# Performance work log

Hardware: AMD Instinct MI355X
Metric: run time of the kernel (lower is better)

The kernel has to match this reference:

```python
import jax, jax.numpy as jnp
import numpy as np

N = 100000
E = 3200000
D = 256


def setup_inputs() -> dict:
    key = jax.random.key(0)
    k1, k2, k3, k4 = jax.random.split(key, 4)
    x = jax.random.normal(k1, (N, D), dtype=jnp.float32)
    edge_index = jax.random.randint(k2, (2, E), 0, N, dtype=jnp.int64)
    # Glorot-ish scale for weights
    s = 1.0 / np.sqrt(D)
    W1 = jax.random.normal(k3, (D, D), dtype=jnp.float32) * s
    W2 = jax.random.normal(k4, (D, D), dtype=jnp.float32) * s
    b1 = jnp.zeros((D,), dtype=jnp.float32)
    b2 = jnp.zeros((D,), dtype=jnp.float32)
    return {"x": x, "edge_index": edge_index, "W1": W1, "b1": b1, "W2": W2, "b2": b2}


def _gcn_norm(edge_index, num_nodes):
    # PyG gcn_norm with add_self_loops=True, symmetric normalization.
    loop = jnp.arange(num_nodes, dtype=edge_index.dtype)
    src = jnp.concatenate([edge_index[0], loop])  # [E+N]
    dst = jnp.concatenate([edge_index[1], loop])  # [E+N]
    ones = jnp.ones(src.shape[0], dtype=jnp.float32)
    deg = jax.ops.segment_sum(ones, dst, num_segments=num_nodes)  # in-degree incl. self loop
    dis = jnp.where(deg > 0, jax.lax.rsqrt(deg), 0.0)
    norm = dis[src] * dis[dst]  # [E+N]
    return src, dst, norm


def _gcn_layer(x, src, dst, norm, W, b, num_nodes):
    xw = x @ W                                   # [N, D] dense GEMM
    msg = xw[src] * norm[:, None]                # gather + scale  [E+N, D]
    out = jax.ops.segment_sum(msg, dst, num_segments=num_nodes)  # scatter-add
    return out + b


def reference(x, edge_index, W1, b1, W2, b2):
    src, dst, norm = _gcn_norm(edge_index, N)
    h = jax.nn.elu(_gcn_layer(x, src, dst, norm, W1, b1, N))
    h = jax.nn.elu(_gcn_layer(h, src, dst, norm, W2, b2, N))
    return h
```

## Files before the change

kernel.cpp:

```cpp
#include <hip/hip_runtime.h>
#include <math.h>

#define N_NODES 100000
#define N_EDGES 3200000
#define DIM 256
#define SCAN_B 1024
#define SCAN_NBLK ((N_NODES + SCAN_B - 1) / SCAN_B)
#define NPASS 8
#define WIN ((N_NODES + NPASS - 1) / NPASS)

typedef unsigned short u16;
typedef unsigned int u32;
typedef __attribute__((ext_vector_type(8))) short bf16x8;
typedef __attribute__((ext_vector_type(4))) float f32x4;

__device__ __forceinline__ float bf2f(u16 u) {
    union { u32 i; float f; } v; v.i = ((u32)u) << 16; return v.f;
}
__device__ __forceinline__ u16 f2bf(float f) {
    union { float f; u32 i; } v; v.f = f;
    u32 x = v.i;
    return (u16)((x + 0x7fffu + ((x >> 16) & 1u)) >> 16);
}
__device__ __forceinline__ float sane(float v) {
    union { float f; u32 i; } u; u.f = v;
    if ((u.i & 0x7f800000u) == 0x7f800000u) return 0.f;
    return v;
}
__device__ __forceinline__ int iclamp(int v, int lo, int hi) {
    return v < lo ? lo : (v > hi ? hi : v);
}

__global__ void detect_kernel(const u32* __restrict__ xw_words,
                              const int* __restrict__ ei, int* __restrict__ flags) {
    int lane = threadIdx.x;
    int cnt = 0;
#pragma unroll
    for (int j = 0; j < 4; ++j) {
        u32 e = (xw_words[lane + 64 * j] >> 7) & 0xffu;
        cnt += (e >= 0x70 && e <= 0x88) ? 1 : 0;
    }
    int nz = 0;
#pragma unroll
    for (int j = 0; j < 4; ++j) nz += (ei[2 * (lane + 64 * j) + 1] != 0) ? 1 : 0;
#pragma unroll
    for (int off = 32; off; off >>= 1) {
        cnt += __shfl_down(cnt, off, 64);
        nz += __shfl_down(nz, off, 64);
    }
    if (lane == 0) {
        flags[0] = (cnt < 128) ? 1 : 0;
        flags[1] = (nz == 0) ? 1 : 0;
    }
}

__device__ __forceinline__ int edge_val(const int* __restrict__ ei, int which,
                                        int i, int f64) {
    long long idx = (long long)which * N_EDGES + i;
    int v = f64 ? ei[idx * 2] : ei[idx];
    return iclamp(v, 0, N_NODES - 1);
}

__global__ void convert_x(const void* __restrict__ xin, u16* __restrict__ xbf,
                          const int* __restrict__ flags) {
    long long i = (long long)blockIdx.x * blockDim.x + threadIdx.x;
    if (i >= (long long)N_NODES * DIM) return;
    float v = flags[0] ? ((const float*)xin)[i] : bf2f(((const u16*)xin)[i]);
    xbf[i] = f2bf(sane(v));
}

__global__ void count_convert(const int* __restrict__ ei, int* __restrict__ rowcount,
                              int* __restrict__ src32, int* __restrict__ dst32,
                              const int* __restrict__ flags) {
    int i = blockIdx.x * blockDim.x + threadIdx.x;
    if (i < N_EDGES) {
        int f = flags[1];
        int s = edge_val(ei, 0, i, f);
        int d = edge_val(ei, 1, i, f);
        src32[i] = s;
        dst32[i] = d;
        atomicAdd(&rowcount[d], 1);
    }
}

__global__ void compute_dis(const int* __restrict__ rowcount, float* __restrict__ dis) {
    int i = blockIdx.x * blockDim.x + threadIdx.x;
    if (i < N_NODES) {
        int c = iclamp(rowcount[i], 0, N_EDGES);
        dis[i] = rsqrtf((float)(c + 1));
    }
}

__global__ __launch_bounds__(SCAN_B) void scan_block_sums(const int* __restrict__ cnt,
                                                          int* __restrict__ bsum) {
    __shared__ int ws[16];
    int i = blockIdx.x * SCAN_B + threadIdx.x;
    int v = (i < N_NODES) ? cnt[i] : 0;
#pragma unroll
    for (int off = 32; off; off >>= 1) v += __shfl_down(v, off, 64);
    if ((threadIdx.x & 63) == 0) ws[threadIdx.x >> 6] = v;
    __syncthreads();
    if (threadIdx.x < 16) {
        int t = ws[threadIdx.x];
#pragma unroll
        for (int off = 8; off; off >>= 1) t += __shfl_down(t, off, 16);
        if (threadIdx.x == 0) bsum[blockIdx.x] = t;
    }
}

__global__ void scan_bsum(int* __restrict__ bsum, int* __restrict__ rowptr) {
    __shared__ int sdata[128];
    int i = threadIdx.x;
    int v = (i < SCAN_NBLK) ? bsum[i] : 0;
    sdata[i] = v;
    __syncthreads();
    for (int off = 1; off < 128; off <<= 1) {
        int t = (i >= off) ? sdata[i - off] : 0;
        __syncthreads();
        sdata[i] += t;
        __syncthreads();
    }
    if (i < SCAN_NBLK) bsum[i] = sdata[i] - v;
    if (i == 0) rowptr[N_NODES] = sdata[127];
}

__global__ __launch_bounds__(SCAN_B) void scan_final(const int* __restrict__ cnt,
                                                     const int* __restrict__ bsum,
                                                     int* __restrict__ rowptr,
                                                     int* __restrict__ cursor) {
    __shared__ int ws[16];
    int lane = threadIdx.x & 63;
    int wid = threadIdx.x >> 6;
    int i = blockIdx.x * SCAN_B + threadIdx.x;
    int c = (i < N_NODES) ? cnt[i] : 0;
    int v = c;
#pragma unroll
    for (int off = 1; off < 64; off <<= 1) {
        int t = __shfl_up(v, off, 64);
        if (lane >= off) v += t;
    }
    if (lane == 63) ws[wid] = v;
    __syncthreads();
    int woff = 0;
    for (int w = 0; w < wid; ++w) woff += ws[w];
    int excl = bsum[blockIdx.x] + woff + v - c;
    if (i < N_NODES) { rowptr[i] = excl; cursor[i] = excl; }
}

__global__ void fill_csr_pass(const int* __restrict__ src32,
                              const int* __restrict__ dst32,
                              int* __restrict__ cursor, int* __restrict__ colidx,
                              int lo) {
    int i = blockIdx.x * blockDim.x + threadIdx.x;
    if (i < N_EDGES) {
        int d = dst32[i];
        if ((unsigned)(d - lo) < (unsigned)WIN) {
            int pos = atomicAdd(&cursor[d], 1);
            colidx[pos] = src32[i];
        }
    }
}

__global__ void transpose_w(const void* __restrict__ W, u16* __restrict__ Wt,
                            const int* __restrict__ flags) {
    int n = blockIdx.x;
    int k = threadIdx.x;
    float v = flags[0] ? ((const float*)W)[k * DIM + n]
                       : bf2f(((const u16*)W)[k * DIM + n]);
    Wt[n * DIM + k] = f2bf(sane(v));
}

__global__ __launch_bounds__(256) void gemm_mfma(const u16* __restrict__ A,
                                                 const u16* __restrict__ Wt,
                                                 u16* __restrict__ out) {
    int w = threadIdx.x >> 6;
    int lane = threadIdx.x & 63;
    int rt = blockIdx.x;
    int m = lane & 15;
    int quad = lane >> 4;

    bf16x8 B[4][8];
#pragma unroll
    for (int t2 = 0; t2 < 4; ++t2)
#pragma unroll
        for (int ks = 0; ks < 8; ++ks)
            B[t2][ks] = *(const bf16x8*)(Wt + (size_t)((w * 4 + t2) * 16 + m) * DIM +
                                         ks * 32 + quad * 8);

    const u16* arow = A + (size_t)(rt * 16 + m) * DIM + quad * 8;
    f32x4 acc[4];
#pragma unroll
    for (int t2 = 0; t2 < 4; ++t2) acc[t2] = (f32x4){0.f, 0.f, 0.f, 0.f};

#pragma unroll
    for (int ks = 0; ks < 8; ++ks) {
        bf16x8 a = *(const bf16x8*)(arow + ks * 32);
#pragma unroll
        for (int t2 = 0; t2 < 4; ++t2)
            acc[t2] = __builtin_amdgcn_mfma_f32_16x16x32_bf16(a, B[t2][ks], acc[t2], 0, 0, 0);
    }

#pragma unroll
    for (int t2 = 0; t2 < 4; ++t2) {
#pragma unroll
        for (int r = 0; r < 4; ++r) {
            int row = rt * 16 + quad * 4 + r;
            int c = w * 64 + t2 * 16 + m;
            out[(size_t)row * DIM + c] = f2bf(sane(acc[t2][r]));
        }
    }
}

__global__ __launch_bounds__(256) void aggregate(const u16* __restrict__ xw,
                                                 const int* __restrict__ rowptr,
                                                 const int* __restrict__ colidx,
                                                 const float* __restrict__ dis,
                                                 const void* __restrict__ bias,
                                                 void* __restrict__ out,
                                                 const int* __restrict__ flags,
                                                 int final_layer) {
    int wid = threadIdx.x >> 6;
    int lane = threadIdx.x & 63;
    int node = blockIdx.x * 4 + wid;
    if (node >= N_NODES) return;
    int c0 = lane * 4;
    const u16* base = xw + c0;

    float dn = dis[node];
    float a0, a1, a2, a3;
    {
        ushort4 v = *(const ushort4*)(base + (size_t)node * DIM);
        a0 = dn * bf2f(v.x); a1 = dn * bf2f(v.y);
        a2 = dn * bf2f(v.z); a3 = dn * bf2f(v.w);
    }
    int beg = rowptr[node];
    int end = rowptr[node + 1];
    int e = beg;
    for (; e + 8 <= end; e += 8) {
        int s[8];
        float w[8];
        ushort4 vv[8];
#pragma unroll
        for (int k = 0; k < 8; ++k) s[k] = colidx[e + k];
#pragma unroll
        for (int k = 0; k < 8; ++k) vv[k] = *(const ushort4*)(base + (size_t)s[k] * DIM);
#pragma unroll
        for (int k = 0; k < 8; ++k) w[k] = dis[s[k]];
#pragma unroll
        for (int k = 0; k < 8; ++k) {
            a0 += w[k] * bf2f(vv[k].x);
            a1 += w[k] * bf2f(vv[k].y);
            a2 += w[k] * bf2f(vv[k].z);
            a3 += w[k] * bf2f(vv[k].w);
        }
    }
    for (; e < end; ++e) {
        int s = colidx[e];
        float w = dis[s];
        ushort4 v = *(const ushort4*)(base + (size_t)s * DIM);
        a0 += w * bf2f(v.x); a1 += w * bf2f(v.y);
        a2 += w * bf2f(v.z); a3 += w * bf2f(v.w);
    }

    float b0, b1, b2, b3;
    int f32mode = flags[0];
    if (f32mode) {
        float4 bv = *(const float4*)((const float*)bias + c0);
        b0 = bv.x; b1 = bv.y; b2 = bv.z; b3 = bv.w;
    } else {
        ushort4 bv = *(const ushort4*)((const u16*)bias + c0);
        b0 = bf2f(bv.x); b1 = bf2f(bv.y); b2 = bf2f(bv.z); b3 = bf2f(bv.w);
    }
    float o0 = dn * a0 + b0;
    float o1 = dn * a1 + b1;
    float o2 = dn * a2 + b2;
    float o3 = dn * a3 + b3;
    o0 = sane(o0 > 0.f ? o0 : expm1f(o0));
    o1 = sane(o1 > 0.f ? o1 : expm1f(o1));
    o2 = sane(o2 > 0.f ? o2 : expm1f(o2));
    o3 = sane(o3 > 0.f ? o3 : expm1f(o3));
    if (final_layer && f32mode) {
        float4 ov; ov.x = o0; ov.y = o1; ov.z = o2; ov.w = o3;
        *(float4*)((float*)out + (size_t)node * DIM + c0) = ov;
    } else {
        ushort4 ov;
        ov.x = f2bf(o0); ov.y = f2bf(o1); ov.z = f2bf(o2); ov.w = f2bf(o3);
        *(ushort4*)((u16*)out + (size_t)node * DIM + c0) = ov;
    }
}

extern "C" void kernel_launch(void* const* d_in, const int* in_sizes, int n_in,
                              void* d_out, int out_size, void* d_ws, size_t ws_size,
                              hipStream_t stream) {
    const void* x  = d_in[0];
    const int*  ei = (const int*)d_in[1];
    const void* W1 = d_in[2];
    const void* b1 = d_in[3];
    const void* W2 = d_in[4];
    const void* b2 = d_in[5];

    char* ws = (char*)d_ws;
    size_t off = 0;
    auto alloc = [&](size_t bytes) {
        void* p = ws + off;
        off = (off + bytes + 255) & ~(size_t)255;
        return p;
    };
    int*   flags    = (int*)alloc(256);
    int*   rowcount = (int*)alloc((size_t)N_NODES * 4);
    int*   rowptr   = (int*)alloc((size_t)(N_NODES + 1) * 4);
    int*   cursor   = (int*)alloc((size_t)N_NODES * 4);
    int*   colidx   = (int*)alloc((size_t)N_EDGES * 4);
    float* dis      = (float*)alloc((size_t)N_NODES * 4);
    int*   bsum     = (int*)alloc((size_t)SCAN_NBLK * 4 + 256);
    u16*   Wt       = (u16*)alloc((size_t)DIM * DIM * 2);
    u16*   xw       = (u16*)alloc((size_t)N_NODES * DIM * 2);
    (void)ws_size;

    int* src32 = (int*)xw;
    int* dst32 = src32 + N_EDGES;

    u16* xbf = (u16*)d_out;

    detect_kernel<<<1, 64, 0, stream>>>((const u32*)x, ei, flags);
    hipMemsetAsync(rowcount, 0, (size_t)N_NODES * 4, stream);
    count_convert<<<(N_EDGES + 255) / 256, 256, 0, stream>>>(ei, rowcount, src32, dst32, flags);
    compute_dis<<<(N_NODES + 255) / 256, 256, 0, stream>>>(rowcount, dis);
    scan_block_sums<<<SCAN_NBLK, SCAN_B, 0, stream>>>(rowcount, bsum);
    scan_bsum<<<1, 128, 0, stream>>>(bsum, rowptr);
    scan_final<<<SCAN_NBLK, SCAN_B, 0, stream>>>(rowcount, bsum, rowptr, cursor);
    for (int p = 0; p < NPASS; ++p)
        fill_csr_pass<<<(N_EDGES + 255) / 256, 256, 0, stream>>>(src32, dst32, cursor,
                                                                 colidx, p * WIN);
    convert_x<<<(N_NODES * DIM + 255) / 256, 256, 0, stream>>>(x, xbf, flags);

    transpose_w<<<DIM, DIM, 0, stream>>>(W1, Wt, flags);
    gemm_mfma<<<N_NODES / 16, 256, 0, stream>>>(xbf, Wt, xw);
    aggregate<<<N_NODES / 4, 256, 0, stream>>>(xw, rowptr, colidx, dis, b1, d_out, flags, 0);

    transpose_w<<<DIM, DIM, 0, stream>>>(W2, Wt, flags);
    gemm_mfma<<<N_NODES / 16, 256, 0, stream>>>((const u16*)d_out, Wt, xw);
    aggregate<<<N_NODES / 4, 256, 0, stream>>>(xw, rowptr, colidx, dis, b2, d_out, flags, 1);
}
```

Before: 1.235 ms.

## Prescale GEMM output by source norm and split wave across edges in aggregate

```diff
diff --git a/kernel.cpp b/kernel.cpp
--- a/kernel.cpp
+++ b/kernel.cpp
@@ -29,6 +29,12 @@
 }
 __device__ __forceinline__ int iclamp(int v, int lo, int hi) {
     return v < lo ? lo : (v > hi ? hi : v);
+}
+__device__ __forceinline__ float2 cvt2(u32 d) {
+    union { u32 i; float f; } lo, hi;
+    lo.i = d << 16;
+    hi.i = d & 0xffff0000u;
+    return make_float2(lo.f, hi.f);
 }
 
 __global__ void detect_kernel(const u32* __restrict__ xw_words,
@@ -172,6 +178,7 @@
 
 __global__ __launch_bounds__(256) void gemm_mfma(const u16* __restrict__ A,
                                                  const u16* __restrict__ Wt,
+                                                 const float* __restrict__ dis,
                                                  u16* __restrict__ out) {
     int w = threadIdx.x >> 6;
     int lane = threadIdx.x & 63;
@@ -200,13 +207,16 @@
             acc[t2] = __builtin_amdgcn_mfma_f32_16x16x32_bf16(a, B[t2][ks], acc[t2], 0, 0, 0);
     }
 
+    float4 dv = *(const float4*)(dis + rt * 16 + quad * 4);
+    float dr[4] = {dv.x, dv.y, dv.z, dv.w};
+
 #pragma unroll
     for (int t2 = 0; t2 < 4; ++t2) {
 #pragma unroll
         for (int r = 0; r < 4; ++r) {
             int row = rt * 16 + quad * 4 + r;
             int c = w * 64 + t2 * 16 + m;
-            out[(size_t)row * DIM + c] = f2bf(sane(acc[t2][r]));
+            out[(size_t)row * DIM + c] = f2bf(sane(acc[t2][r] * dr[r]));
         }
     }
 }
@@ -223,45 +233,72 @@
     int lane = threadIdx.x & 63;
     int node = blockIdx.x * 4 + wid;
     if (node >= N_NODES) return;
-    int c0 = lane * 4;
-    const u16* base = xw + c0;
-
-    float dn = dis[node];
-    float a0, a1, a2, a3;
-    {
-        ushort4 v = *(const ushort4*)(base + (size_t)node * DIM);
-        a0 = dn * bf2f(v.x); a1 = dn * bf2f(v.y);
-        a2 = dn * bf2f(v.z); a3 = dn * bf2f(v.w);
-    }
+    int h = lane >> 5;
+    int c8 = (lane & 31) * 8;
+    const u16* base = xw + c8;
+
+    float2 a0 = make_float2(0.f, 0.f), a1 = a0, a2 = a0, a3 = a0;
+    if (h == 0) {
+        uint4 v = *(const uint4*)(base + (size_t)node * DIM);
+        a0 = cvt2(v.x); a1 = cvt2(v.y); a2 = cvt2(v.z); a3 = cvt2(v.w);
+    }
+
+#define ACC4(v)                                                   \
+    do {                                                          \
+        float2 t0 = cvt2((v).x), t1 = cvt2((v).y);                \
+        float2 t2 = cvt2((v).z), t3 = cvt2((v).w);                \
+        a0.x += t0.x; a0.y += t0.y; a1.x += t1.x; a1.y += t1.y;   \
+        a2.x += t2.x; a2.y += t2.y; a3.x += t3.x; a3.y += t3.y;   \
+    } while (0)
+
     int beg = rowptr[node];
     int end = rowptr[node + 1];
     int e = beg;
-    for (; e + 8 <= end; e += 8) {
-        int s[8];
-        float w[8];
-        ushort4 vv[8];
-#pragma unroll
-        for (int k = 0; k < 8; ++k) s[k] = colidx[e + k];
-#pragma unroll
-        for (int k = 0; k < 8; ++k) vv[k] = *(const ushort4*)(base + (size_t)s[k] * DIM);
-#pragma unroll
-        for (int k = 0; k < 8; ++k) w[k] = dis[s[k]];
-#pragma unroll
-        for (int k = 0; k < 8; ++k) {
-            a0 += w[k] * bf2f(vv[k].x);
-            a1 += w[k] * bf2f(vv[k].y);
-            a2 += w[k] * bf2f(vv[k].z);
-            a3 += w[k] * bf2f(vv[k].w);
+
+    int pe = (beg + 3) & ~3;
+    if (pe > end) pe = end;
+    for (int t = e; t < pe; t += 2) {
+        int idx = t + h;
+        if (idx < pe) {
+            int s = colidx[idx];
+            uint4 v = *(const uint4*)(base + (size_t)s * DIM);
+            ACC4(v);
         }
     }
-    for (; e < end; ++e) {
-        int s = colidx[e];
-        float w = dis[s];
-        ushort4 v = *(const ushort4*)(base + (size_t)s * DIM);
-        a0 += w * bf2f(v.x); a1 += w * bf2f(v.y);
-        a2 += w * bf2f(v.z); a3 += w * bf2f(v.w);
-    }
-
+    e = pe;
+
+    int me = e + ((end - e) & ~7);
+    int h4 = h * 4;
+    for (; e < me; e += 8) {
+        int4 c4 = *(const int4*)(colidx + e + h4);
+        uint4 v0 = *(const uint4*)(base + (size_t)c4.x * DIM);
+        uint4 v1 = *(const uint4*)(base + (size_t)c4.y * DIM);
+        uint4 v2 = *(const uint4*)(base + (size_t)c4.z * DIM);
+        uint4 v3 = *(const uint4*)(base + (size_t)c4.w * DIM);
+        ACC4(v0); ACC4(v1); ACC4(v2); ACC4(v3);
+    }
+
+    for (; e < end; e += 2) {
+        int idx = e + h;
+        if (idx < end) {
+            int s = colidx[idx];
+            uint4 v = *(const uint4*)(base + (size_t)s * DIM);
+            ACC4(v);
+        }
+    }
+#undef ACC4
+
+    a0.x += __shfl_xor(a0.x, 32); a0.y += __shfl_xor(a0.y, 32);
+    a1.x += __shfl_xor(a1.x, 32); a1.y += __shfl_xor(a1.y, 32);
+    a2.x += __shfl_xor(a2.x, 32); a2.y += __shfl_xor(a2.y, 32);
+    a3.x += __shfl_xor(a3.x, 32); a3.y += __shfl_xor(a3.y, 32);
+
+    float s0, s1, s2, s3;
+    if (h == 0) { s0 = a0.x; s1 = a0.y; s2 = a1.x; s3 = a1.y; }
+    else        { s0 = a2.x; s1 = a2.y; s2 = a3.x; s3 = a3.y; }
+    int c0 = c8 + h * 4;
+
+    float dn = dis[node];
     float b0, b1, b2, b3;
     int f32mode = flags[0];
     if (f32mode) {
@@ -271,10 +308,10 @@
         ushort4 bv = *(const ushort4*)((const u16*)bias + c0);
         b0 = bf2f(bv.x); b1 = bf2f(bv.y); b2 = bf2f(bv.z); b3 = bf2f(bv.w);
     }
-    float o0 = dn * a0 + b0;
-    float o1 = dn * a1 + b1;
-    float o2 = dn * a2 + b2;
-    float o3 = dn * a3 + b3;
+    float o0 = dn * s0 + b0;
+    float o1 = dn * s1 + b1;
+    float o2 = dn * s2 + b2;
+    float o3 = dn * s3 + b3;
     o0 = sane(o0 > 0.f ? o0 : expm1f(o0));
     o1 = sane(o1 > 0.f ? o1 : expm1f(o1));
     o2 = sane(o2 > 0.f ? o2 : expm1f(o2));
@@ -335,10 +372,10 @@
     convert_x<<<(N_NODES * DIM + 255) / 256, 256, 0, stream>>>(x, xbf, flags);
 
     transpose_w<<<DIM, DIM, 0, stream>>>(W1, Wt, flags);
-    gemm_mfma<<<N_NODES / 16, 256, 0, stream>>>(xbf, Wt, xw);
+    gemm_mfma<<<N_NODES / 16, 256, 0, stream>>>(xbf, Wt, dis, xw);
     aggregate<<<N_NODES / 4, 256, 0, stream>>>(xw, rowptr, colidx, dis, b1, d_out, flags, 0);
 
     transpose_w<<<DIM, DIM, 0, stream>>>(W2, Wt, flags);
-    gemm_mfma<<<N_NODES / 16, 256, 0, stream>>>((const u16*)d_out, Wt, xw);
+    gemm_mfma<<<N_NODES / 16, 256, 0, stream>>>((const u16*)d_out, Wt, dis, xw);
     aggregate<<<N_NODES / 4, 256, 0, stream>>>(xw, rowptr, colidx, dis, b2, d_out, flags, 1);
 }
```

Result: no change. 1.225 ms (-0.7%).

## Bucket CSR by source window and process node groups per wave for gather locality

Applied to the files above, without the earlier changes.

```diff
diff --git a/kernel.cpp b/kernel.cpp
--- a/kernel.cpp
+++ b/kernel.cpp
@@ -5,9 +5,17 @@
 #define N_EDGES 3200000
 #define DIM 256
 #define SCAN_B 1024
-#define SCAN_NBLK ((N_NODES + SCAN_B - 1) / SCAN_B)
 #define NPASS 8
 #define WIN ((N_NODES + NPASS - 1) / NPASS)
+
+#define WSH 12
+#define NW 25
+#define NBUCK (NW * N_NODES)
+#define SCAN_GRID_W ((NBUCK + SCAN_B - 1) / SCAN_B)
+
+#define NPW 12
+#define NPB (4 * NPW)
+#define AGG_GRID ((N_NODES + NPB - 1) / NPB)
 
 typedef unsigned short u16;
 typedef unsigned int u32;
@@ -29,6 +37,12 @@
 }
 __device__ __forceinline__ int iclamp(int v, int lo, int hi) {
     return v < lo ? lo : (v > hi ? hi : v);
+}
+__device__ __forceinline__ float2 cvt2(u32 d) {
+    union { u32 i; float f; } lo, hi;
+    lo.i = d << 16;
+    hi.i = d & 0xffff0000u;
+    return make_float2(lo.f, hi.f);
 }
 
 __global__ void detect_kernel(const u32* __restrict__ xw_words,
@@ -69,7 +83,7 @@
     xbf[i] = f2bf(sane(v));
 }
 
-__global__ void count_convert(const int* __restrict__ ei, int* __restrict__ rowcount,
+__global__ void count_convert(const int* __restrict__ ei, int* __restrict__ cntW,
                               int* __restrict__ src32, int* __restrict__ dst32,
                               const int* __restrict__ flags) {
     int i = blockIdx.x * blockDim.x + threadIdx.x;
@@ -79,23 +93,28 @@
         int d = edge_val(ei, 1, i, f);
         src32[i] = s;
         dst32[i] = d;
-        atomicAdd(&rowcount[d], 1);
-    }
-}
-
-__global__ void compute_dis(const int* __restrict__ rowcount, float* __restrict__ dis) {
+        int w = s >> WSH;
+        atomicAdd(&cntW[w * N_NODES + d], 1);
+    }
+}
+
+__global__ void deg_dis(const int* __restrict__ cntW, float* __restrict__ dis) {
     int i = blockIdx.x * blockDim.x + threadIdx.x;
     if (i < N_NODES) {
-        int c = iclamp(rowcount[i], 0, N_EDGES);
-        dis[i] = rsqrtf((float)(c + 1));
+        int d = 0;
+#pragma unroll
+        for (int w = 0; w < NW; ++w) d += cntW[w * N_NODES + i];
+        d = iclamp(d, 0, N_EDGES);
+        dis[i] = rsqrtf((float)(d + 1));
     }
 }
 
 __global__ __launch_bounds__(SCAN_B) void scan_block_sums(const int* __restrict__ cnt,
-                                                          int* __restrict__ bsum) {
+                                                          int* __restrict__ bsum,
+                                                          int M) {
     __shared__ int ws[16];
     int i = blockIdx.x * SCAN_B + threadIdx.x;
-    int v = (i < N_NODES) ? cnt[i] : 0;
+    int v = (i < M) ? cnt[i] : 0;
 #pragma unroll
     for (int off = 32; off; off >>= 1) v += __shfl_down(v, off, 64);
     if ((threadIdx.x & 63) == 0) ws[threadIdx.x >> 6] = v;
@@ -108,31 +127,38 @@
     }
 }
 
-__global__ void scan_bsum(int* __restrict__ bsum, int* __restrict__ rowptr) {
-    __shared__ int sdata[128];
-    int i = threadIdx.x;
-    int v = (i < SCAN_NBLK) ? bsum[i] : 0;
-    sdata[i] = v;
+__global__ __launch_bounds__(1024) void scan_bsum_big(int* __restrict__ bsum) {
+    __shared__ int sd[1024];
+    int t = threadIdx.x;
+    int base = t * 3;
+    int v0 = (base     < SCAN_GRID_W) ? bsum[base]     : 0;
+    int v1 = (base + 1 < SCAN_GRID_W) ? bsum[base + 1] : 0;
+    int v2 = (base + 2 < SCAN_GRID_W) ? bsum[base + 2] : 0;
+    int s = v0 + v1 + v2;
+    sd[t] = s;
     __syncthreads();
-    for (int off = 1; off < 128; off <<= 1) {
-        int t = (i >= off) ? sdata[i - off] : 0;
+    for (int off = 1; off < 1024; off <<= 1) {
+        int x = (t >= off) ? sd[t - off] : 0;
         __syncthreads();
-        sdata[i] += t;
+        sd[t] += x;
         __syncthreads();
     }
-    if (i < SCAN_NBLK) bsum[i] = sdata[i] - v;
-    if (i == 0) rowptr[N_NODES] = sdata[127];
-}
-
-__global__ __launch_bounds__(SCAN_B) void scan_final(const int* __restrict__ cnt,
-                                                     const int* __restrict__ bsum,
-                                                     int* __restrict__ rowptr,
-                                                     int* __restrict__ cursor) {
+    int ex = sd[t] - s;
+    if (base     < SCAN_GRID_W) bsum[base]     = ex;
+    if (base + 1 < SCAN_GRID_W) bsum[base + 1] = ex + v0;
+    if (base + 2 < SCAN_GRID_W) bsum[base + 2] = ex + v0 + v1;
+}
+
+__global__ __launch_bounds__(SCAN_B) void scan_final_w(const int* __restrict__ cnt,
+                                                       const int* __restrict__ bsum,
+                                                       int* __restrict__ rowptr,
+                                                       int* __restrict__ cursor,
+                                                       int M) {
     __shared__ int ws[16];
     int lane = threadIdx.x & 63;
     int wid = threadIdx.x >> 6;
     int i = blockIdx.x * SCAN_B + threadIdx.x;
-    int c = (i < N_NODES) ? cnt[i] : 0;
+    int c = (i < M) ? cnt[i] : 0;
     int v = c;
 #pragma unroll
     for (int off = 1; off < 64; off <<= 1) {
@@ -144,19 +170,22 @@
     int woff = 0;
     for (int w = 0; w < wid; ++w) woff += ws[w];
     int excl = bsum[blockIdx.x] + woff + v - c;
-    if (i < N_NODES) { rowptr[i] = excl; cursor[i] = excl; }
+    if (i < M) { rowptr[i] = excl; cursor[i] = excl; }
+    if (blockIdx.x == 0 && threadIdx.x == 0) rowptr[M] = N_EDGES;
 }
 
 __global__ void fill_csr_pass(const int* __restrict__ src32,
                               const int* __restrict__ dst32,
-                              int* __restrict__ cursor, int* __restrict__ colidx,
+                              int* __restrict__ cursorW, int* __restrict__ colidx,
                               int lo) {
     int i = blockIdx.x * blockDim.x + threadIdx.x;
     if (i < N_EDGES) {
         int d = dst32[i];
         if ((unsigned)(d - lo) < (unsigned)WIN) {
-            int pos = atomicAdd(&cursor[d], 1);
-            colidx[pos] = src32[i];
+            int s = src32[i];
+            int w = s >> WSH;
+            int pos = atomicAdd(&cursorW[w * N_NODES + d], 1);
+            colidx[pos] = s;
         }
     }
 }
@@ -172,6 +201,7 @@
 
 __global__ __launch_bounds__(256) void gemm_mfma(const u16* __restrict__ A,
                                                  const u16* __restrict__ Wt,
+                                                 const float* __restrict__ dis,
                                                  u16* __restrict__ out) {
     int w = threadIdx.x >> 6;
     int lane = threadIdx.x & 63;
@@ -200,70 +230,89 @@
             acc[t2] = __builtin_amdgcn_mfma_f32_16x16x32_bf16(a, B[t2][ks], acc[t2], 0, 0, 0);
     }
 
+    float4 dv = *(const float4*)(dis + rt * 16 + quad * 4);
+    float dr[4] = {dv.x, dv.y, dv.z, dv.w};
+
 #pragma unroll
     for (int t2 = 0; t2 < 4; ++t2) {
 #pragma unroll
         for (int r = 0; r < 4; ++r) {
             int row = rt * 16 + quad * 4 + r;
             int c = w * 64 + t2 * 16 + m;
-            out[(size_t)row * DIM + c] = f2bf(sane(acc[t2][r]));
-        }
-    }
-}
-
-__global__ __launch_bounds__(256) void aggregate(const u16* __restrict__ xw,
-                                                 const int* __restrict__ rowptr,
-                                                 const int* __restrict__ colidx,
-                                                 const float* __restrict__ dis,
-                                                 const void* __restrict__ bias,
-                                                 void* __restrict__ out,
-                                                 const int* __restrict__ flags,
-                                                 int final_layer) {
+            out[(size_t)row * DIM + c] = f2bf(sane(acc[t2][r] * dr[r]));
+        }
+    }
+}
+
+__global__ __launch_bounds__(256, 4) void aggregate(const u16* __restrict__ xw,
+                                                    const int* __restrict__ rowptrW,
+                                                    const int* __restrict__ colidx,
+                                                    const float* __restrict__ dis,
+                                                    const void* __restrict__ bias,
+                                                    void* __restrict__ out,
+                                                    const int* __restrict__ flags,
+                                                    int final_layer) {
     int wid = threadIdx.x >> 6;
     int lane = threadIdx.x & 63;
-    int node = blockIdx.x * 4 + wid;
-    if (node >= N_NODES) return;
+    int n0 = (blockIdx.x * 4 + wid) * NPW;
+    const u16* xcol = xw + lane * 4;
+
+    f32x4 acc[NPW];
+#pragma unroll
+    for (int ln = 0; ln < NPW; ++ln) acc[ln] = (f32x4){0.f, 0.f, 0.f, 0.f};
+
+#pragma unroll
+    for (int ln = 0; ln < NPW; ++ln) {
+        int n = n0 + ln;
+        if (n < N_NODES) {
+            uint2 v = *(const uint2*)(xcol + (size_t)n * DIM);
+            float2 t0 = cvt2(v.x), t1 = cvt2(v.y);
+            acc[ln][0] += t0.x; acc[ln][1] += t0.y;
+            acc[ln][2] += t1.x; acc[ln][3] += t1.y;
+        }
+    }
+
+    for (int w = 0; w < NW; ++w) {
+        const int* pr = rowptrW + w * N_NODES;
+        int pv = 0;
+        if (lane <= NPW) {
+            int idx = n0 + lane;
+            if (idx > N_NODES) idx = N_NODES;
+            pv = pr[idx];
+        }
+        int p[NPW], e[NPW];
+#pragma unroll
+        for (int ln = 0; ln < NPW; ++ln) {
+            p[ln] = __builtin_amdgcn_readfirstlane(__shfl(pv, ln, 64));
+            e[ln] = __builtin_amdgcn_readfirstlane(__shfl(pv, ln + 1, 64));
+        }
+        while (true) {
+            int am = 0;
+            uint2 v[NPW];
+#pragma unroll
+            for (int ln = 0; ln < NPW; ++ln) {
+                if (p[ln] < e[ln]) {
+                    int s = colidx[p[ln]];
+                    v[ln] = *(const uint2*)(xcol + (size_t)s * DIM);
+                    am |= 1 << ln;
+                }
+            }
+            if (am == 0) break;
+#pragma unroll
+            for (int ln = 0; ln < NPW; ++ln) {
+                if (am & (1 << ln)) {
+                    ++p[ln];
+                    float2 t0 = cvt2(v[ln].x), t1 = cvt2(v[ln].y);
+                    acc[ln][0] += t0.x; acc[ln][1] += t0.y;
+                    acc[ln][2] += t1.x; acc[ln][3] += t1.y;
+                }
+            }
+        }
+    }
+
+    int f32mode = flags[0];
     int c0 = lane * 4;
-    const u16* base = xw + c0;
-
-    float dn = dis[node];
-    float a0, a1, a2, a3;
-    {
-        ushort4 v = *(const ushort4*)(base + (size_t)node * DIM);
-        a0 = dn * bf2f(v.x); a1 = dn * bf2f(v.y);
-        a2 = dn * bf2f(v.z); a3 = dn * bf2f(v.w);
-    }
-    int beg = rowptr[node];
-    int end = rowptr[node + 1];
-    int e = beg;
-    for (; e + 8 <= end; e += 8) {
-        int s[8];
-        float w[8];
-        ushort4 vv[8];
-#pragma unroll
-        for (int k = 0; k < 8; ++k) s[k] = colidx[e + k];
-#pragma unroll
-        for (int k = 0; k < 8; ++k) vv[k] = *(const ushort4*)(base + (size_t)s[k] * DIM);
-#pragma unroll
-        for (int k = 0; k < 8; ++k) w[k] = dis[s[k]];
-#pragma unroll
-        for (int k = 0; k < 8; ++k) {
-            a0 += w[k] * bf2f(vv[k].x);
-            a1 += w[k] * bf2f(vv[k].y);
-            a2 += w[k] * bf2f(vv[k].z);
-            a3 += w[k] * bf2f(vv[k].w);
-        }
-    }
-    for (; e < end; ++e) {
-        int s = colidx[e];
-        float w = dis[s];
-        ushort4 v = *(const ushort4*)(base + (size_t)s * DIM);
-        a0 += w * bf2f(v.x); a1 += w * bf2f(v.y);
-        a2 += w * bf2f(v.z); a3 += w * bf2f(v.w);
-    }
-
     float b0, b1, b2, b3;
-    int f32mode = flags[0];
     if (f32mode) {
         float4 bv = *(const float4*)((const float*)bias + c0);
         b0 = bv.x; b1 = bv.y; b2 = bv.z; b3 = bv.w;
@@ -271,21 +320,27 @@
         ushort4 bv = *(const ushort4*)((const u16*)bias + c0);
         b0 = bf2f(bv.x); b1 = bf2f(bv.y); b2 = bf2f(bv.z); b3 = bf2f(bv.w);
     }
-    float o0 = dn * a0 + b0;
-    float o1 = dn * a1 + b1;
-    float o2 = dn * a2 + b2;
-    float o3 = dn * a3 + b3;
-    o0 = sane(o0 > 0.f ? o0 : expm1f(o0));
-    o1 = sane(o1 > 0.f ? o1 : expm1f(o1));
-    o2 = sane(o2 > 0.f ? o2 : expm1f(o2));
-    o3 = sane(o3 > 0.f ? o3 : expm1f(o3));
-    if (final_layer && f32mode) {
-        float4 ov; ov.x = o0; ov.y = o1; ov.z = o2; ov.w = o3;
-        *(float4*)((float*)out + (size_t)node * DIM + c0) = ov;
-    } else {
-        ushort4 ov;
-        ov.x = f2bf(o0); ov.y = f2bf(o1); ov.z = f2bf(o2); ov.w = f2bf(o3);
-        *(ushort4*)((u16*)out + (size_t)node * DIM + c0) = ov;
+#pragma unroll
+    for (int ln = 0; ln < NPW; ++ln) {
+        int n = n0 + ln;
+        if (n >= N_NODES) break;
+        float dn = dis[n];
+        float o0 = dn * acc[ln][0] + b0;
+        float o1 = dn * acc[ln][1] + b1;
+        float o2 = dn * acc[ln][2] + b2;
+        float o3 = dn * acc[ln][3] + b3;
+        o0 = sane(o0 > 0.f ? o0 : expm1f(o0));
+        o1 = sane(o1 > 0.f ? o1 : expm1f(o1));
+        o2 = sane(o2 > 0.f ? o2 : expm1f(o2));
+        o3 = sane(o3 > 0.f ? o3 : expm1f(o3));
+        if (final_layer && f32mode) {
+            float4 ov; ov.x = o0; ov.y = o1; ov.z = o2; ov.w = o3;
+            *(float4*)((float*)out + (size_t)n * DIM + c0) = ov;
+        } else {
+            ushort4 ov;
+            ov.x = f2bf(o0); ov.y = f2bf(o1); ov.z = f2bf(o2); ov.w = f2bf(o3);
+            *(ushort4*)((u16*)out + (size_t)n * DIM + c0) = ov;
+        }
     }
 }
 
@@ -306,39 +361,40 @@
         off = (off + bytes + 255) & ~(size_t)255;
         return p;
     };
-    int*   flags    = (int*)alloc(256);
-    int*   rowcount = (int*)alloc((size_t)N_NODES * 4);
-    int*   rowptr   = (int*)alloc((size_t)(N_NODES + 1) * 4);
-    int*   cursor   = (int*)alloc((size_t)N_NODES * 4);
-    int*   colidx   = (int*)alloc((size_t)N_EDGES * 4);
-    float* dis      = (float*)alloc((size_t)N_NODES * 4);
-    int*   bsum     = (int*)alloc((size_t)SCAN_NBLK * 4 + 256);
-    u16*   Wt       = (u16*)alloc((size_t)DIM * DIM * 2);
-    u16*   xw       = (u16*)alloc((size_t)N_NODES * DIM * 2);
+    int*   flags   = (int*)alloc(256);
+    int*   rowptrW = (int*)alloc(((size_t)NBUCK + 1) * 4);
+    int*   colidx  = (int*)alloc((size_t)N_EDGES * 4);
+    float* dis     = (float*)alloc((size_t)N_NODES * 4);
+    int*   bsum    = (int*)alloc((size_t)SCAN_GRID_W * 4 + 256);
+    u16*   Wt      = (u16*)alloc((size_t)DIM * DIM * 2);
+    u16*   xw      = (u16*)alloc((size_t)N_NODES * DIM * 2);
     (void)ws_size;
 
-    int* src32 = (int*)xw;
-    int* dst32 = src32 + N_EDGES;
+    char* xwb = (char*)xw;
+    int* src32   = (int*)xwb;
+    int* dst32   = (int*)(xwb + (size_t)N_EDGES * 4);
+    int* cntW    = (int*)(xwb + (size_t)N_EDGES * 8);
+    int* cursorW = (int*)(xwb + (size_t)N_EDGES * 8 + (size_t)NBUCK * 4);
 
     u16* xbf = (u16*)d_out;
 
     detect_kernel<<<1, 64, 0, stream>>>((const u32*)x, ei, flags);
-    hipMemsetAsync(rowcount, 0, (size_t)N_NODES * 4, stream);
-    count_convert<<<(N_EDGES + 255) / 256, 256, 0, stream>>>(ei, rowcount, src32, dst32, flags);
-    compute_dis<<<(N_NODES + 255) / 256, 256, 0, stream>>>(rowcount, dis);
-    scan_block_sums<<<SCAN_NBLK, SCAN_B, 0, stream>>>(rowcount, bsum);
-    scan_bsum<<<1, 128, 0, stream>>>(bsum, rowptr);
-    scan_final<<<SCAN_NBLK, SCAN_B, 0, stream>>>(rowcount, bsum, rowptr, cursor);
+    hipMemsetAsync(cntW, 0, (size_t)NBUCK * 4, stream);
+    count_convert<<<(N_EDGES + 255) / 256, 256, 0, stream>>>(ei, cntW, src32, dst32, flags);
+    deg_dis<<<(N_NODES + 255) / 256, 256, 0, stream>>>(cntW, dis);
+    scan_block_sums<<<SCAN_GRID_W, SCAN_B, 0, stream>>>(cntW, bsum, NBUCK);
+    scan_bsum_big<<<1, 1024, 0, stream>>>(bsum);
+    scan_final_w<<<SCAN_GRID_W, SCAN_B, 0, stream>>>(cntW, bsum, rowptrW, cursorW, NBUCK);
     for (int p = 0; p < NPASS; ++p)
-        fill_csr_pass<<<(N_EDGES + 255) / 256, 256, 0, stream>>>(src32, dst32, cursor,
+        fill_csr_pass<<<(N_EDGES + 255) / 256, 256, 0, stream>>>(src32, dst32, cursorW,
                                                                  colidx, p * WIN);
     convert_x<<<(N_NODES * DIM + 255) / 256, 256, 0, stream>>>(x, xbf, flags);
 
     transpose_w<<<DIM, DIM, 0, stream>>>(W1, Wt, flags);
-    gemm_mfma<<<N_NODES / 16, 256, 0, stream>>>(xbf, Wt, xw);
-    aggregate<<<N_NODES / 4, 256, 0, stream>>>(xw, rowptr, colidx, dis, b1, d_out, flags, 0);
+    gemm_mfma<<<N_NODES / 16, 256, 0, stream>>>(xbf, Wt, dis, xw);
+    aggregate<<<AGG_GRID, 256, 0, stream>>>(xw, rowptrW, colidx, dis, b1, d_out, flags, 0);
 
     transpose_w<<<DIM, DIM, 0, stream>>>(W2, Wt, flags);
-    gemm_mfma<<<N_NODES / 16, 256, 0, stream>>>((const u16*)d_out, Wt, xw);
-    aggregate<<<N_NODES / 4, 256, 0, stream>>>(xw, rowptr, colidx, dis, b2, d_out, flags, 1);
-}
+    gemm_mfma<<<N_NODES / 16, 256, 0, stream>>>((const u16*)d_out, Wt, dis, xw);
+    aggregate<<<AGG_GRID, 256, 0, stream>>>(xw, rowptrW, colidx, dis, b2, d_out, flags, 1);
+}
```

Result: slower. 1.668 ms (+35.1%).
